# Kernel optimization log

Hardware: AMD Instinct MI355X
Metric: run time of the kernel (lower is better)

The kernel has to match this reference:

```python
import jax, jax.numpy as jnp
import numpy as np

B, T, DIM = 2, 2048, 2048
N_HEADS, N_KV_HEADS = 16, 4
HEAD_DIM = DIM // N_HEADS  # 128
N_REP = N_HEADS // N_KV_HEADS  # 4
ROPE_THETA = 10000.0


def setup_inputs() -> dict:
    key = jax.random.key(0)
    ks = jax.random.split(key, 5)
    x = jax.random.normal(ks[0], (B, T, DIM), dtype=jnp.float32)
    # RoPE tables (equivalent to complex freqs_cis = exp(i * t * inv_freq))
    inv_freq = 1.0 / (ROPE_THETA ** (np.arange(0, HEAD_DIM, 2, dtype=np.float32) / HEAD_DIM))
    t = np.arange(T, dtype=np.float32)
    ang = np.outer(t, inv_freq)  # (T, HEAD_DIM//2)
    freqs_cos = jnp.asarray(np.cos(ang), dtype=jnp.float32)
    freqs_sin = jnp.asarray(np.sin(ang), dtype=jnp.float32)
    s = 0.02
    wq = jax.random.normal(ks[1], (DIM, N_HEADS * HEAD_DIM), dtype=jnp.float32) * s
    wk = jax.random.normal(ks[2], (DIM, N_KV_HEADS * HEAD_DIM), dtype=jnp.float32) * s
    wv = jax.random.normal(ks[3], (DIM, N_KV_HEADS * HEAD_DIM), dtype=jnp.float32) * s
    wo = jax.random.normal(ks[4], (N_HEADS * HEAD_DIM, DIM), dtype=jnp.float32) * s
    return {"x": x, "freqs_cos": freqs_cos, "freqs_sin": freqs_sin,
            "wq": wq, "wk": wk, "wv": wv, "wo": wo}


def _apply_rope(t, cos, sin):
    # t: (B, H, T, hd); cos/sin: (T, hd//2); interleaved pairs like view_as_complex
    tr = t[..., 0::2]
    ti = t[..., 1::2]
    c = cos[None, None, :, :]
    s = sin[None, None, :, :]
    out_r = tr * c - ti * s
    out_i = tr * s + ti * c
    return jnp.stack([out_r, out_i], axis=-1).reshape(t.shape)


def reference(x, freqs_cos, freqs_sin, wq, wk, wv, wo):
    Bb, Tt, C = x.shape
    q = (x @ wq).reshape(Bb, Tt, N_HEADS, HEAD_DIM).transpose(0, 2, 1, 3)      # (B,H,T,hd)
    k = (x @ wk).reshape(Bb, Tt, N_KV_HEADS, HEAD_DIM).transpose(0, 2, 1, 3)   # (B,KV,T,hd)
    v = (x @ wv).reshape(Bb, Tt, N_KV_HEADS, HEAD_DIM).transpose(0, 2, 1, 3)
    q = _apply_rope(q, freqs_cos[:Tt], freqs_sin[:Tt])
    k = _apply_rope(k, freqs_cos[:Tt], freqs_sin[:Tt])
    # GQA repeat_kv
    k = jnp.repeat(k, N_REP, axis=1)  # (B,H,T,hd)
    v = jnp.repeat(v, N_REP, axis=1)
    scale = 1.0 / jnp.sqrt(jnp.float32(HEAD_DIM))
    scores = jnp.einsum("bhqd,bhkd->bhqk", q, k) * scale
    causal = jnp.tril(jnp.ones((Tt, Tt), dtype=bool))
    scores = jnp.where(causal[None, None], scores, jnp.float32(-jnp.inf))
    attn = jax.nn.softmax(scores, axis=-1)
    out = jnp.einsum("bhqk,bhkd->bhqd", attn, v)          # (B,H,T,hd)
    out = out.transpose(0, 2, 1, 3).reshape(Bb, Tt, C)
    return out @ wo
```

## Files before the change

kernel.cpp:

```cpp
#include <hip/hip_runtime.h>
#include <hip/hip_bf16.h>

#define SEQT 2048
#define NH 16
#define HD 128

typedef __bf16 bf16;
typedef __bf16 bf16x4 __attribute__((ext_vector_type(4)));
typedef __bf16 bf16x8 __attribute__((ext_vector_type(8)));
typedef float f32x4 __attribute__((ext_vector_type(4)));
typedef float f32x16 __attribute__((ext_vector_type(16)));

__device__ inline void glds16(const bf16* g, bf16* l) {
  __builtin_amdgcn_global_load_lds(
      (const __attribute__((address_space(1))) unsigned int*)g,
      (__attribute__((address_space(3))) unsigned int*)l, 16, 0, 0);
}

__device__ inline unsigned int cvtpk(float a, float b) {
  unsigned int d;
  asm("v_cvt_pk_bf16_f32 %0, %1, %2" : "=v"(d) : "v"(a), "v"(b));
  return d;
}

__global__ __launch_bounds__(256) void k_convert(const float* __restrict__ in,
                                                 bf16* __restrict__ out, int n8) {
  int i = blockIdx.x * 256 + threadIdx.x;
  if (i >= n8) return;
  const float4* p = (const float4*)in + (size_t)i * 2;
  float4 a = p[0], b = p[1];
  bf16x8 o;
  o[0] = (bf16)a.x; o[1] = (bf16)a.y; o[2] = (bf16)a.z; o[3] = (bf16)a.w;
  o[4] = (bf16)b.x; o[5] = (bf16)b.y; o[6] = (bf16)b.z; o[7] = (bf16)b.w;
  *((bf16x8*)out + i) = o;
}

__global__ __launch_bounds__(256) void k_transpose(const float* __restrict__ in,
                                                   bf16* __restrict__ out, int R, int C) {
  __shared__ float tile[32][33];
  int c0 = blockIdx.x * 32, r0 = blockIdx.y * 32;
  int tx = threadIdx.x, ty = threadIdx.y;
#pragma unroll
  for (int i = 0; i < 4; i++)
    tile[ty + i * 8][tx] = in[(size_t)(r0 + ty + i * 8) * C + c0 + tx];
  __syncthreads();
#pragma unroll
  for (int i = 0; i < 4; i++) {
    int r = ty + i * 8;
    out[(size_t)(c0 + r) * R + r0 + tx] = (bf16)tile[tx][r];
  }
}

__global__ __launch_bounds__(256) void k_transpose3(const float* __restrict__ wq,
                                                    const float* __restrict__ wk,
                                                    const float* __restrict__ wv,
                                                    bf16* __restrict__ W) {
  __shared__ float tile[32][33];
  int bx = blockIdx.x;
  const float* src;
  bf16* dst;
  int C;
  if (bx < 64) {
    src = wq; dst = W; C = 2048;
  } else if (bx < 80) {
    src = wk; dst = W + 2048 * 2048; C = 512; bx -= 64;
  } else {
    src = wv; dst = W + 2560 * 2048; C = 512; bx -= 80;
  }
  int c0 = bx * 32, r0 = blockIdx.y * 32;
  int tx = threadIdx.x, ty = threadIdx.y;
#pragma unroll
  for (int i = 0; i < 4; i++)
    tile[ty + i * 8][tx] = src[(size_t)(r0 + ty + i * 8) * C + c0 + tx];
  __syncthreads();
#pragma unroll
  for (int i = 0; i < 4; i++) {
    int r = ty + i * 8;
    dst[(size_t)(c0 + r) * 2048 + r0 + tx] = (bf16)tile[tx][r];
  }
}

__global__ __launch_bounds__(256) void k_transpose4(const float* __restrict__ wq,
                                                    const float* __restrict__ wk,
                                                    const float* __restrict__ wv,
                                                    const float* __restrict__ wo,
                                                    bf16* __restrict__ W,
                                                    bf16* __restrict__ WOT) {
  __shared__ float tile[32][33];
  int bx = blockIdx.x;
  const float* src;
  bf16* dst;
  int C;
  if (bx < 64) {
    src = wq; dst = W; C = 2048;
  } else if (bx < 80) {
    src = wk; dst = W + 2048 * 2048; C = 512; bx -= 64;
  } else if (bx < 96) {
    src = wv; dst = W + 2560 * 2048; C = 512; bx -= 80;
  } else {
    src = wo; dst = WOT; C = 2048; bx -= 96;
  }
  int c0 = bx * 32, r0 = blockIdx.y * 32;
  int tx = threadIdx.x, ty = threadIdx.y;
#pragma unroll
  for (int i = 0; i < 4; i++)
    tile[ty + i * 8][tx] = src[(size_t)(r0 + ty + i * 8) * C + c0 + tx];
  __syncthreads();
#pragma unroll
  for (int i = 0; i < 4; i++) {
    int r = ty + i * 8;
    dst[(size_t)(c0 + r) * 2048 + r0 + tx] = (bf16)tile[tx][r];
  }
}

template <typename OutT>
__global__ __launch_bounds__(512, 2) void k_gemm8(const bf16* __restrict__ A,
                                                  const bf16* __restrict__ Bt,
                                                  OutT* __restrict__ C,
                                                  int nbx, int K, int ldc) {
  __shared__ bf16 AB[2][2][16384];
  int nb = gridDim.x;
  int cpx = nb >> 3;
  int bid = blockIdx.x;
  int sw = (bid & 7) * cpx + (bid >> 3);
  int bx = sw % nbx, by = sw / nbx;
  int m0 = by << 8, n0 = bx << 8;
  int tid = threadIdx.x;
  int lane = tid & 63, wid = tid >> 6;
  int wr2 = wid >> 2, wc2 = wid & 3;
  int lr = lane & 15, lg = lane >> 4;
  int lx = lr & 7;

  f32x4 acc[2][4][2][2] = {};

  int srow = tid >> 3;
  int ssl8 = ((tid & 7) ^ (srow & 7)) * 8;

#define STAGE(SBUF, SAB, SHALF, KO)                                           \
  {                                                                           \
    int ko = (KO) <= (K - 64) ? (KO) : 0;                                     \
    const bf16* gb = (SAB) ? Bt : A;                                          \
    int rb = ((SAB) ? n0 : m0) + (SHALF) * 128 + srow;                        \
    glds16(gb + (size_t)rb * K + ko + ssl8,                                   \
           &AB[SBUF][SAB][(SHALF) * 8192 + tid * 8]);                         \
    glds16(gb + (size_t)(rb + 64) * K + ko + ssl8,                            \
           &AB[SBUF][SAB][(SHALF) * 8192 + (512 + tid) * 8]);                 \
  }

#define PHASE(BUF, QM, QN, SBUF, SAB, SHALF, SKO, DOVM)                       \
  {                                                                           \
    bf16x8 af[4][2], bq[2][2];                                                \
    _Pragma("unroll") for (int mi = 0; mi < 4; mi++)                          \
      _Pragma("unroll") for (int kk = 0; kk < 2; kk++)                        \
        af[mi][kk] = *(const bf16x8*)&AB[BUF][0][                             \
            ((QM) * 128 + wr2 * 64 + mi * 16 + lr) * 64 +                     \
            (((kk * 4 + lg) ^ lx) * 8)];                                      \
    _Pragma("unroll") for (int ni = 0; ni < 2; ni++)                          \
      _Pragma("unroll") for (int kk = 0; kk < 2; kk++)                        \
        bq[ni][kk] = *(const bf16x8*)&AB[BUF][1][                             \
            ((QN) * 128 + wc2 * 32 + ni * 16 + lr) * 64 +                     \
            (((kk * 4 + lg) ^ lx) * 8)];                                      \
    STAGE(SBUF, SAB, SHALF, SKO)                                              \
    if (DOVM) { asm volatile("s_waitcnt vmcnt(4)" ::: "memory"); }            \
    __builtin_amdgcn_sched_barrier(0);                                        \
    __builtin_amdgcn_s_barrier();                                             \
    __builtin_amdgcn_sched_barrier(0);                                        \
    __builtin_amdgcn_s_setprio(1);                                            \
    _Pragma("unroll") for (int kk = 0; kk < 2; kk++)                          \
      _Pragma("unroll") for (int mi = 0; mi < 4; mi++)                        \
        _Pragma("unroll") for (int ni = 0; ni < 2; ni++)                      \
          acc[QM][mi][QN][ni] = __builtin_amdgcn_mfma_f32_16x16x32_bf16(      \
              af[mi][kk], bq[ni][kk], acc[QM][mi][QN][ni], 0, 0, 0);          \
    __builtin_amdgcn_s_setprio(0);                                            \
    __builtin_amdgcn_sched_barrier(0);                                        \
    __builtin_amdgcn_s_barrier();                                             \
    __builtin_amdgcn_sched_barrier(0);                                        \
  }

  STAGE(0, 0, 0, 0) STAGE(0, 1, 0, 0) STAGE(0, 0, 1, 0) STAGE(0, 1, 1, 0)
  STAGE(1, 0, 0, 64) STAGE(1, 1, 0, 64)
  asm volatile("s_waitcnt vmcnt(4)" ::: "memory");
  __builtin_amdgcn_sched_barrier(0);
  __builtin_amdgcn_s_barrier();
  __builtin_amdgcn_sched_barrier(0);

  int nit = K >> 7;
  for (int it = 0; it < nit; it++) {
    int kb = it << 7;
    PHASE(0, 0, 0,  1, 0, 1, kb + 64,  0)
    PHASE(0, 0, 1,  1, 1, 1, kb + 64,  0)
    PHASE(0, 1, 0,  0, 0, 0, kb + 128, 0)
    PHASE(0, 1, 1,  0, 1, 0, kb + 128, 1)
    PHASE(1, 0, 0,  0, 0, 1, kb + 128, 0)
    PHASE(1, 0, 1,  0, 1, 1, kb + 128, 0)
    PHASE(1, 1, 0,  1, 0, 0, kb + 192, 0)
    PHASE(1, 1, 1,  1, 1, 0, kb + 192, 1)
  }
#undef PHASE
#undef STAGE

  int crow = m0 + wr2 * 64 + lg * 4;
  int ccol = n0 + wc2 * 32 + lr;
#pragma unroll
  for (int qm = 0; qm < 2; qm++)
#pragma unroll
    for (int mi = 0; mi < 4; mi++)
#pragma unroll
      for (int qn = 0; qn < 2; qn++)
#pragma unroll
        for (int ni = 0; ni < 2; ni++)
#pragma unroll
          for (int r = 0; r < 4; r++)
            C[(size_t)(crow + qm * 128 + mi * 16 + r) * ldc +
              ccol + qn * 128 + ni * 16] = (OutT)acc[qm][mi][qn][ni][r];
}

template <typename OutT>
__global__ __launch_bounds__(512, 2) void k_gemm8n(const bf16* __restrict__ A,
                                                   const bf16* __restrict__ Bt,
                                                   OutT* __restrict__ C,
                                                   int nbx, int K, int ldc) {
  __shared__ bf16 Al[2][16384];
  __shared__ bf16 Bl[2][8192];
  int nb = gridDim.x;
  int cpx = nb >> 3;
  int bid = blockIdx.x;
  int sw = (bid & 7) * cpx + (bid >> 3);
  int bx = sw % nbx, by = sw / nbx;
  int m0 = by << 8, n0 = bx << 7;
  int tid = threadIdx.x;
  int lane = tid & 63, wid = tid >> 6;
  int wr2 = wid >> 2, wc2 = wid & 3;
  int lr = lane & 15, lg = lane >> 4;
  int lx = lr & 7;

  f32x4 acc[2][4][2] = {};

  int srow = tid >> 3;
  int ssl8 = ((tid & 7) ^ (srow & 7)) * 8;

#define STAGEA(SBUF, SHALF, KO)                                               \
  {                                                                           \
    int ko = (KO) <= (K - 64) ? (KO) : 0;                                     \
    int rb = m0 + (SHALF) * 128 + srow;                                       \
    glds16(A + (size_t)rb * K + ko + ssl8,                                    \
           &Al[SBUF][(SHALF) * 8192 + tid * 8]);                              \
    glds16(A + (size_t)(rb + 64) * K + ko + ssl8,                             \
           &Al[SBUF][(SHALF) * 8192 + (512 + tid) * 8]);                      \
  }
#define STAGEB(SBUF, SHALF, KO)                                               \
  {                                                                           \
    int ko = (KO) <= (K - 64) ? (KO) : 0;                                     \
    int rb = n0 + (SHALF) * 64 + srow;                                        \
    glds16(Bt + (size_t)rb * K + ko + ssl8,                                   \
           &Bl[SBUF][(SHALF) * 4096 + tid * 8]);                              \
  }

#define PHASEN(BUF, QM, QN, STG, DOVM)                                        \
  {                                                                           \
    bf16x8 af[4][2], bq[2];                                                   \
    _Pragma("unroll") for (int mi = 0; mi < 4; mi++)                          \
      _Pragma("unroll") for (int kk = 0; kk < 2; kk++)                        \
        af[mi][kk] = *(const bf16x8*)&Al[BUF][                                \
            (QM) * 8192 + (wr2 * 64 + mi * 16 + lr) * 64 +                    \
            (((kk * 4 + lg) ^ lx) * 8)];                                      \
    _Pragma("unroll") for (int kk = 0; kk < 2; kk++)                          \
      bq[kk] = *(const bf16x8*)&Bl[BUF][                                      \
          (QN) * 4096 + (wc2 * 16 + lr) * 64 + (((kk * 4 + lg) ^ lx) * 8)];   \
    STG                                                                       \
    if (DOVM) { asm volatile("s_waitcnt vmcnt(3)" ::: "memory"); }            \
    __builtin_amdgcn_sched_barrier(0);                                        \
    __builtin_amdgcn_s_barrier();                                             \
    __builtin_amdgcn_sched_barrier(0);                                        \
    __builtin_amdgcn_s_setprio(1);                                            \
    _Pragma("unroll") for (int kk = 0; kk < 2; kk++)                          \
      _Pragma("unroll") for (int mi = 0; mi < 4; mi++)                        \
        acc[QM][mi][QN] = __builtin_amdgcn_mfma_f32_16x16x32_bf16(            \
            af[mi][kk], bq[kk], acc[QM][mi][QN], 0, 0, 0);                    \
    __builtin_amdgcn_s_setprio(0);                                            \
    __builtin_amdgcn_sched_barrier(0);                                        \
    __builtin_amdgcn_s_barrier();                                             \
    __builtin_amdgcn_sched_barrier(0);                                        \
  }

  STAGEA(0, 0, 0) STAGEA(0, 1, 0) STAGEB(0, 0, 0) STAGEB(0, 1, 0)
  STAGEA(1, 0, 64) STAGEB(1, 0, 64)
  asm volatile("s_waitcnt vmcnt(3)" ::: "memory");
  __builtin_amdgcn_sched_barrier(0);
  __builtin_amdgcn_s_barrier();
  __builtin_amdgcn_sched_barrier(0);

  int nit = K >> 7;
  for (int it = 0; it < nit; it++) {
    int kb = it << 7;
    PHASEN(0, 0, 0, STAGEA(1, 1, kb + 64),  0)
    PHASEN(0, 0, 1, STAGEB(1, 1, kb + 64),  0)
    PHASEN(0, 1, 0, STAGEA(0, 0, kb + 128), 0)
    PHASEN(0, 1, 1, STAGEB(0, 0, kb + 128), 1)
    PHASEN(1, 0, 0, STAGEA(0, 1, kb + 128), 0)
    PHASEN(1, 0, 1, STAGEB(0, 1, kb + 128), 0)
    PHASEN(1, 1, 0, STAGEA(1, 0, kb + 192), 0)
    PHASEN(1, 1, 1, STAGEB(1, 0, kb + 192), 1)
  }
#undef PHASEN
#undef STAGEB
#undef STAGEA

  int crow = m0 + wr2 * 64 + lg * 4;
  int ccol = n0 + wc2 * 16 + lr;
#pragma unroll
  for (int qm = 0; qm < 2; qm++)
#pragma unroll
    for (int mi = 0; mi < 4; mi++)
#pragma unroll
      for (int qn = 0; qn < 2; qn++)
#pragma unroll
        for (int r = 0; r < 4; r++)
          C[(size_t)(crow + qm * 128 + mi * 16 + r) * ldc +
            ccol + qn * 64] = (OutT)acc[qm][mi][qn][r];
}

__global__ __launch_bounds__(256, 2) void k_attn(const bf16* __restrict__ qkv,
                                                 bf16* __restrict__ attout,
                                                 const float* __restrict__ fcos,
                                                 const float* __restrict__ fsin) {
  __shared__ bf16 Kl[2][8192];
  __shared__ bf16 Vt[2][128][72];
  __shared__ float Tabs[4][4][32];
  int bid = blockIdx.x;
  int qt = 31 - (bid >> 5);
  int bh = bid & 31;
  int b = bh >> 4, h = bh & 15, kvh = h >> 2;
  int tid = threadIdx.x, wid = tid >> 6, lane = tid & 63;
  int kvhalf = wid >> 1, wq = wid & 1;
  int li = lane & 31, hi = lane >> 5;
  int q0 = qt * 64;
  int qmin = q0 + wq * 32, qmax = qmin + 31;
  int qlane = qmin + li;
  const float C1 = 0.12751744979927212f;

  const bf16* kgbase = qkv + (size_t)b * SEQT * 3072 + 2048 + kvh * HD;
  const bf16* vgbase = kgbase + 512;

  bf16x8 qf[8];
  {
    const bf16* qb = qkv + (size_t)(b * SEQT + qlane) * 3072 + h * HD + hi * 8;
    const float* cb = fcos + qlane * 64 + hi * 4;
    const float* sb = fsin + qlane * 64 + hi * 4;
#pragma unroll
    for (int ks = 0; ks < 8; ks++) {
      bf16x8 v = *(const bf16x8*)(qb + ks * 16);
      f32x4 c = *(const f32x4*)(cb + ks * 8);
      f32x4 s = *(const f32x4*)(sb + ks * 8);
#pragma unroll
      for (int j = 0; j < 4; j++) {
        float a = (float)v[2 * j], bb = (float)v[2 * j + 1];
        qf[ks][2 * j]     = (bf16)(a * c[j] - bb * s[j]);
        qf[ks][2 * j + 1] = (bf16)(a * s[j] + bb * c[j]);
      }
    }
  }

  float mrun = -INFINITY, lpart = 0.f;
  f32x16 o0 = {}, o1 = {}, o2 = {}, o3 = {};
  int nkt = qt + 1;
  int kvbase = 32 * kvhalf;

  int kslot = tid & 15;
  int krow0 = tid >> 4;
  int kphys8 = ((kslot ^ krow0) & 15) * 8;

  int g = (lane >> 4) & 3;
  int lr = lane & 15;
  int kq4 = (wid * 4 + g) * 4;
  int dc = lr * 8;
  int xr = (lr & 7) << 3;
  int kvw = kq4 ^ xr;

  bf16x8 krg[4];
  f32x4 ck[4], sk[4];
  bf16x8 vr0, vr1, vr2, vr3;

#pragma unroll
  for (int r = 0; r < 4; r++) {
    int row = r * 16 + krow0;
    krg[r] = *(const bf16x8*)(kgbase + (size_t)row * 3072 + kslot * 8);
    ck[r] = *(const f32x4*)(fcos + (size_t)row * 64 + kslot * 4);
    sk[r] = *(const f32x4*)(fsin + (size_t)row * 64 + kslot * 4);
  }
  {
    const bf16* vrow = vgbase + (size_t)kq4 * 3072 + dc;
    vr0 = *(const bf16x8*)(vrow);
    vr1 = *(const bf16x8*)(vrow + 3072);
    vr2 = *(const bf16x8*)(vrow + 6144);
    vr3 = *(const bf16x8*)(vrow + 9216);
  }

  for (int kt = 0; kt < nkt; kt++) {
    int cur = kt & 1;
    int kv0 = kt * 64;
    asm volatile("s_waitcnt vmcnt(0)" ::: "memory");

#pragma unroll
    for (int r = 0; r < 4; r++) {
      bf16x8 kw;
#pragma unroll
      for (int j = 0; j < 4; j++) {
        float a = (float)krg[r][2 * j], bb = (float)krg[r][2 * j + 1];
        kw[2 * j]     = (bf16)(a * ck[r][j] - bb * sk[r][j]);
        kw[2 * j + 1] = (bf16)(a * sk[r][j] + bb * ck[r][j]);
      }
      *(bf16x8*)&Kl[cur][(r * 16 + krow0) * 128 + kphys8] = kw;
    }

#pragma unroll
    for (int j = 0; j < 8; j++) {
      bf16x4 w;
      w[0] = vr0[j]; w[1] = vr1[j]; w[2] = vr2[j]; w[3] = vr3[j];
      *(bf16x4*)&Vt[cur][dc + j][kvw] = w;
    }

    asm volatile("s_waitcnt lgkmcnt(0)" ::: "memory");
    __builtin_amdgcn_sched_barrier(0);
    __builtin_amdgcn_s_barrier();
    __builtin_amdgcn_sched_barrier(0);

    if (kt + 1 < nkt) {
      int kv1 = kv0 + 64;
#pragma unroll
      for (int r = 0; r < 4; r++) {
        int row = kv1 + r * 16 + krow0;
        krg[r] = *(const bf16x8*)(kgbase + (size_t)row * 3072 + kslot * 8);
        ck[r] = *(const f32x4*)(fcos + (size_t)row * 64 + kslot * 4);
        sk[r] = *(const f32x4*)(fsin + (size_t)row * 64 + kslot * 4);
      }
      const bf16* vrow = vgbase + (size_t)(kv1 + kq4) * 3072 + dc;
      vr0 = *(const bf16x8*)(vrow);
      vr1 = *(const bf16x8*)(vrow + 3072);
      vr2 = *(const bf16x8*)(vrow + 6144);
      vr3 = *(const bf16x8*)(vrow + 9216);
    }

    if (kv0 + kvbase <= qmax) {
      f32x16 s0 = {};
      const char* kb0 = (const char*)&Kl[cur][0] + kvhalf * 8192 + li * 256;
      __builtin_amdgcn_s_setprio(1);
#pragma unroll
      for (int ks = 0; ks < 8; ks++) {
        int off = ((ks * 2 + hi) ^ (li & 15)) << 4;
        bf16x8 kf0 = *(const bf16x8*)(kb0 + off);
        s0 = __builtin_amdgcn_mfma_f32_32x32x16_bf16(kf0, qf[ks], s0, 0, 0, 0);
      }
      __builtin_amdgcn_s_setprio(0);

      if (kv0 + kvbase + 31 > qmin) {
        int base0 = kv0 + kvbase + 4 * hi - qlane;
#pragma unroll
        for (int r = 0; r < 16; r++) {
          int off = (r & 3) + 8 * (r >> 2);
          if (base0 + off > 0) s0[r] = -INFINITY;
        }
      }

      float pm = s0[0];
#pragma unroll
      for (int r = 1; r < 16; r++) pm = fmaxf(pm, s0[r]);
      pm = fmaxf(pm, __shfl_xor(pm, 32));

      if (!__all(pm - mrun <= 62.0f)) {
        float mnew = fmaxf(mrun, pm);
        float alpha = exp2f((mrun - mnew) * C1);
        mrun = mnew;
        lpart *= alpha;
        Tabs[0][wid][li] = alpha;
        asm volatile("s_waitcnt lgkmcnt(0)" ::: "memory");
        f32x4 a0 = *(const f32x4*)&Tabs[0][wid][4 * hi];
        f32x4 a1 = *(const f32x4*)&Tabs[0][wid][4 * hi + 8];
        f32x4 a2 = *(const f32x4*)&Tabs[0][wid][4 * hi + 16];
        f32x4 a3 = *(const f32x4*)&Tabs[0][wid][4 * hi + 24];
#define RESC_RR(rr, av)                                            \
  _Pragma("unroll") for (int i = 0; i < 4; i++) {                  \
    float f = av[i];                                               \
    o0[rr * 4 + i] *= f; o1[rr * 4 + i] *= f;                      \
    o2[rr * 4 + i] *= f; o3[rr * 4 + i] *= f;                      \
  }
        RESC_RR(0, a0) RESC_RR(1, a1) RESC_RR(2, a2) RESC_RR(3, a3)
#undef RESC_RR
      }

      float mC = mrun * C1;
      float rs = 0.f;
#pragma unroll
      for (int r = 0; r < 16; r++) {
        float p = exp2f(fmaf(s0[r], C1, -mC));
        s0[r] = p; rs += p;
      }
      lpart += rs;

      union U4 { unsigned int u[4]; bf16x8 v; };
      U4 pa0, pa1;
      {
        unsigned int e0 = cvtpk(s0[0], s0[1]), e1 = cvtpk(s0[2], s0[3]);
        unsigned int e2 = cvtpk(s0[4], s0[5]), e3 = cvtpk(s0[6], s0[7]);
        unsigned int e4 = cvtpk(s0[8], s0[9]), e5 = cvtpk(s0[10], s0[11]);
        unsigned int e6 = cvtpk(s0[12], s0[13]), e7 = cvtpk(s0[14], s0[15]);
        unsigned int t0 = __shfl_xor(e0, 32), t1 = __shfl_xor(e1, 32);
        unsigned int t2 = __shfl_xor(e2, 32), t3 = __shfl_xor(e3, 32);
        unsigned int t4 = __shfl_xor(e4, 32), t5 = __shfl_xor(e5, 32);
        unsigned int t6 = __shfl_xor(e6, 32), t7 = __shfl_xor(e7, 32);
        pa0.u[0] = hi ? t2 : e0;  pa0.u[1] = hi ? t3 : e1;
        pa0.u[2] = hi ? e2 : t0;  pa0.u[3] = hi ? e3 : t1;
        pa1.u[0] = hi ? t6 : e4;  pa1.u[1] = hi ? t7 : e5;
        pa1.u[2] = hi ? e6 : t4;  pa1.u[3] = hi ? e7 : t5;
      }

      __builtin_amdgcn_s_setprio(1);
#define PV_DB(OACC, DB)                                                      \
  {                                                                          \
    int d = DB * 32 + li;                                                    \
    int xv = ((d >> 3) & 7) << 3;                                            \
    bf16x8 vb0 = *(const bf16x8*)&Vt[cur][d][(kvbase + hi * 8) ^ xv];        \
    bf16x8 vb1 = *(const bf16x8*)&Vt[cur][d][(kvbase + 16 + hi * 8) ^ xv];   \
    OACC = __builtin_amdgcn_mfma_f32_32x32x16_bf16(pa0.v, vb0, OACC, 0, 0, 0); \
    OACC = __builtin_amdgcn_mfma_f32_32x32x16_bf16(pa1.v, vb1, OACC, 0, 0, 0); \
  }
      PV_DB(o0, 0) PV_DB(o1, 1) PV_DB(o2, 2) PV_DB(o3, 3)
#undef PV_DB
      __builtin_amdgcn_s_setprio(0);
    }
  }

  lpart += __shfl_xor(lpart, 32);
  Tabs[0][wid][li] = mrun;
  Tabs[1][wid][li] = lpart;
  asm volatile("s_waitcnt lgkmcnt(0)" ::: "memory");
  __builtin_amdgcn_s_barrier();
  int peer = wid ^ 2;
  float mP = Tabs[0][peer][li], lP = Tabs[1][peer][li];
  float mS = fmaxf(mrun, mP);
  float fMe = exp2f((mrun - mS) * C1);
  float fPe = exp2f((mP - mS) * C1);
  float lTot = lpart * fMe + lP * fPe;
  Tabs[2][wid][li] = fMe;
  Tabs[3][wid][li] = 1.f / lTot;
  asm volatile("s_waitcnt lgkmcnt(0)" ::: "memory");
  __builtin_amdgcn_s_barrier();
  f32x4 Fv0 = *(const f32x4*)&Tabs[2][wid][4 * hi];
  f32x4 Fv1 = *(const f32x4*)&Tabs[2][wid][4 * hi + 8];
  f32x4 Fv2 = *(const f32x4*)&Tabs[2][wid][4 * hi + 16];
  f32x4 Fv3 = *(const f32x4*)&Tabs[2][wid][4 * hi + 24];
  f32x4 Iv0 = *(const f32x4*)&Tabs[3][wid][4 * hi];
  f32x4 Iv1 = *(const f32x4*)&Tabs[3][wid][4 * hi + 8];
  f32x4 Iv2 = *(const f32x4*)&Tabs[3][wid][4 * hi + 16];
  f32x4 Iv3 = *(const f32x4*)&Tabs[3][wid][4 * hi + 24];

  float* X = (float*)&Kl[0][0];
  float* Xb = X + (wid & 1) * 4096;
  if (kvhalf == 1) {
#define XW_RR(OACC, DB, rr, Fv)                                              \
  _Pragma("unroll") for (int i = 0; i < 4; i++)                              \
    Xb[(4 * hi + 8 * rr + i) * 128 + DB * 32 + li] = OACC[rr * 4 + i] * Fv[i];
#define XW_DB(OACC, DB) XW_RR(OACC, DB, 0, Fv0) XW_RR(OACC, DB, 1, Fv1) \
                        XW_RR(OACC, DB, 2, Fv2) XW_RR(OACC, DB, 3, Fv3)
    XW_DB(o0, 0) XW_DB(o1, 1) XW_DB(o2, 2) XW_DB(o3, 3)
#undef XW_DB
#undef XW_RR
  }
  asm volatile("s_waitcnt lgkmcnt(0)" ::: "memory");
  __builtin_amdgcn_s_barrier();
  if (kvhalf == 0) {
#define XR_RR(OACC, DB, rr, Fv)                                              \
  _Pragma("unroll") for (int i = 0; i < 4; i++)                              \
    OACC[rr * 4 + i] = OACC[rr * 4 + i] * Fv[i] +                            \
        Xb[(4 * hi + 8 * rr + i) * 128 + DB * 32 + li];
#define XR_DB(OACC, DB) XR_RR(OACC, DB, 0, Fv0) XR_RR(OACC, DB, 1, Fv1) \
                        XR_RR(OACC, DB, 2, Fv2) XR_RR(OACC, DB, 3, Fv3)
    XR_DB(o0, 0) XR_DB(o1, 1) XR_DB(o2, 2) XR_DB(o3, 3)
#undef XR_DB
#undef XR_RR
    size_t obase = (size_t)(b * SEQT) * 2048 + h * HD;
#define STORE_RR(rr, lv)                                                     \
  _Pragma("unroll") for (int i = 0; i < 4; i++) {                            \
    int q = qmin + 4 * hi + 8 * rr + i;                                      \
    size_t rowb = obase + (size_t)q * 2048 + li;                             \
    attout[rowb + 0]  = (bf16)(o0[rr * 4 + i] * lv[i]);                      \
    attout[rowb + 32] = (bf16)(o1[rr * 4 + i] * lv[i]);                      \
    attout[rowb + 64] = (bf16)(o2[rr * 4 + i] * lv[i]);                      \
    attout[rowb + 96] = (bf16)(o3[rr * 4 + i] * lv[i]);                      \
  }
    STORE_RR(0, Iv0) STORE_RR(1, Iv1) STORE_RR(2, Iv2) STORE_RR(3, Iv3)
#undef STORE_RR
  }
}

extern "C" void kernel_launch(void* const* d_in, const int* in_sizes, int n_in,
                              void* d_out, int out_size, void* d_ws, size_t ws_size,
                              hipStream_t stream) {
  const float* x    = (const float*)d_in[0];
  const float* fcos = (const float*)d_in[1];
  const float* fsin = (const float*)d_in[2];
  const float* wq   = (const float*)d_in[3];
  const float* wk   = (const float*)d_in[4];
  const float* wv   = (const float*)d_in[5];
  const float* wo   = (const float*)d_in[6];
  float* out = (float*)d_out;

  char* ws = (char*)d_ws;
  bf16* XB  = (bf16*)ws;
  bf16* W   = (bf16*)(ws + 16777216);
  bf16* QKV = (bf16*)(ws + 16777216 + 12582912);
  bool bigws = ws_size >= 62914560ull;
  bf16* WOT = bigws ? (bf16*)(ws + 54525952) : W;

  dim3 tb(32, 8);
  if (bigws) {
    k_transpose4<<<dim3(160, 64), tb, 0, stream>>>(wq, wk, wv, wo, W, WOT);
  } else {
    k_transpose3<<<dim3(96, 64), tb, 0, stream>>>(wq, wk, wv, W);
  }
  k_convert<<<4096, 256, 0, stream>>>(x, XB, 1048576);
  k_gemm8<bf16><<<192, 512, 0, stream>>>(XB, W, QKV, 12, 2048, 3072);
  k_attn<<<1024, 256, 0, stream>>>(QKV, XB, fcos, fsin);
  if (!bigws) {
    k_transpose<<<dim3(64, 64), tb, 0, stream>>>(wo, W, 2048, 2048);
  }
  k_gemm8n<float><<<256, 512, 0, stream>>>(XB, WOT, out, 16, 2048, 2048);
}
```

Measured before the change: 237.2 us.

## Pre-apply RoPE to K in separate kernel and stream K tiles via global_load_lds

Adds a small kernel that applies RoPE to the K part of the QKV buffer in place, once per key row. The attention kernel then loads K tiles directly into shared memory with swizzled async global-to-LDS loads, double-buffered into the next slot. This removes the RoPE recomputation that every query tile repeated for each K tile, along with the per-thread register staging and cos/sin loads. The cost is an extra kernel launch and one read-modify-write pass over K.

```diff
diff --git a/kernel.cpp b/kernel.cpp
--- a/kernel.cpp
+++ b/kernel.cpp
@@ -320,6 +320,35 @@
             ccol + qn * 64] = (OutT)acc[qm][mi][qn][r];
 }
 
+__global__ __launch_bounds__(256) void k_ropek(bf16* __restrict__ qkv,
+                                               const float* __restrict__ fcos,
+                                               const float* __restrict__ fsin) {
+  int gid = blockIdx.x * 256 + threadIdx.x;
+  int row = gid >> 5;
+  int p = gid & 31;
+  int head = p >> 3;
+  int g8 = p & 7;
+  int t = row & (SEQT - 1);
+  bf16* ptr = qkv + (size_t)row * 3072 + 2048 + head * HD + g8 * 16;
+  bf16x8 v0 = *(const bf16x8*)ptr;
+  bf16x8 v1 = *(const bf16x8*)(ptr + 8);
+  const f32x4* cp = (const f32x4*)(fcos + t * 64 + g8 * 8);
+  const f32x4* sp = (const f32x4*)(fsin + t * 64 + g8 * 8);
+  f32x4 c0 = cp[0], c1 = cp[1], s0 = sp[0], s1 = sp[1];
+  bf16x8 o0, o1;
+#pragma unroll
+  for (int k = 0; k < 4; k++) {
+    float a0 = (float)v0[2 * k], b0 = (float)v0[2 * k + 1];
+    o0[2 * k]     = (bf16)(a0 * c0[k] - b0 * s0[k]);
+    o0[2 * k + 1] = (bf16)(a0 * s0[k] + b0 * c0[k]);
+    float a1 = (float)v1[2 * k], b1 = (float)v1[2 * k + 1];
+    o1[2 * k]     = (bf16)(a1 * c1[k] - b1 * s1[k]);
+    o1[2 * k + 1] = (bf16)(a1 * s1[k] + b1 * c1[k]);
+  }
+  *(bf16x8*)ptr = o0;
+  *(bf16x8*)(ptr + 8) = o1;
+}
+
 __global__ __launch_bounds__(256, 2) void k_attn(const bf16* __restrict__ qkv,
                                                  bf16* __restrict__ attout,
                                                  const float* __restrict__ fcos,
@@ -366,10 +395,6 @@
   int nkt = qt + 1;
   int kvbase = 32 * kvhalf;
 
-  int kslot = tid & 15;
-  int krow0 = tid >> 4;
-  int kphys8 = ((kslot ^ krow0) & 15) * 8;
-
   int g = (lane >> 4) & 3;
   int lr = lane & 15;
   int kq4 = (wid * 4 + g) * 4;
@@ -377,16 +402,14 @@
   int xr = (lr & 7) << 3;
   int kvw = kq4 ^ xr;
 
-  bf16x8 krg[4];
-  f32x4 ck[4], sk[4];
   bf16x8 vr0, vr1, vr2, vr3;
 
 #pragma unroll
   for (int r = 0; r < 4; r++) {
-    int row = r * 16 + krow0;
-    krg[r] = *(const bf16x8*)(kgbase + (size_t)row * 3072 + kslot * 8);
-    ck[r] = *(const f32x4*)(fcos + (size_t)row * 64 + kslot * 4);
-    sk[r] = *(const f32x4*)(fsin + (size_t)row * 64 + kslot * 4);
+    int ci = r * 256 + tid;
+    int row = ci >> 4;
+    int sl = (ci & 15) ^ (row & 15);
+    glds16(kgbase + (size_t)row * 3072 + sl * 8, &Kl[0][ci * 8]);
   }
   {
     const bf16* vrow = vgbase + (size_t)kq4 * 3072 + dc;
@@ -402,18 +425,6 @@
     asm volatile("s_waitcnt vmcnt(0)" ::: "memory");
 
 #pragma unroll
-    for (int r = 0; r < 4; r++) {
-      bf16x8 kw;
-#pragma unroll
-      for (int j = 0; j < 4; j++) {
-        float a = (float)krg[r][2 * j], bb = (float)krg[r][2 * j + 1];
-        kw[2 * j]     = (bf16)(a * ck[r][j] - bb * sk[r][j]);
-        kw[2 * j + 1] = (bf16)(a * sk[r][j] + bb * ck[r][j]);
-      }
-      *(bf16x8*)&Kl[cur][(r * 16 + krow0) * 128 + kphys8] = kw;
-    }
-
-#pragma unroll
     for (int j = 0; j < 8; j++) {
       bf16x4 w;
       w[0] = vr0[j]; w[1] = vr1[j]; w[2] = vr2[j]; w[3] = vr3[j];
@@ -427,12 +438,13 @@
 
     if (kt + 1 < nkt) {
       int kv1 = kv0 + 64;
+      bf16* kdst = &Kl[cur ^ 1][0];
 #pragma unroll
       for (int r = 0; r < 4; r++) {
-        int row = kv1 + r * 16 + krow0;
-        krg[r] = *(const bf16x8*)(kgbase + (size_t)row * 3072 + kslot * 8);
-        ck[r] = *(const f32x4*)(fcos + (size_t)row * 64 + kslot * 4);
-        sk[r] = *(const f32x4*)(fsin + (size_t)row * 64 + kslot * 4);
+        int ci = r * 256 + tid;
+        int row = ci >> 4;
+        int sl = (ci & 15) ^ (row & 15);
+        glds16(kgbase + (size_t)(kv1 + row) * 3072 + sl * 8, kdst + ci * 8);
       }
       const bf16* vrow = vgbase + (size_t)(kv1 + kq4) * 3072 + dc;
       vr0 = *(const bf16x8*)(vrow);
@@ -620,6 +632,7 @@
   }
   k_convert<<<4096, 256, 0, stream>>>(x, XB, 1048576);
   k_gemm8<bf16><<<192, 512, 0, stream>>>(XB, W, QKV, 12, 2048, 3072);
+  k_ropek<<<512, 256, 0, stream>>>(QKV, fcos, fsin);
   k_attn<<<1024, 256, 0, stream>>>(QKV, XB, fcos, fsin);
   if (!bigws) {
     k_transpose<<<dim3(64, 64), tb, 0, stream>>>(wo, W, 2048, 2048);
```

Result: faster. 218.9 us (median of 2 runs) (-7.7%).
